# Kernel optimization log

Hardware: AMD Instinct MI355X
Metric: run time of the kernel (lower is better)

The kernel has to match this reference:

```python
import jax, jax.numpy as jnp
import numpy as np

B, OBS, ACT, NT, E, H1, H2, D = 4096, 390, 20, 10, 8, 1024, 512, 256


def setup_inputs() -> dict:
    key = jax.random.key(0)
    ks = jax.random.split(key, 16)
    f32 = jnp.float32

    def w(k, shape, fan_in):
        return jax.random.normal(k, shape, f32) / np.float32(np.sqrt(fan_in))

    return {
        "state_feat": jax.random.normal(ks[0], (B, OBS), f32),
        "act": jax.random.normal(ks[1], (B, ACT), f32),
        "task_id": jax.random.randint(ks[2], (B,), 0, NT, jnp.int32),
        "rep_W1": w(ks[3], (OBS + ACT, H1), OBS + ACT),
        "rep_b1": jnp.zeros((H1,), f32),
        "rep_W2": w(ks[4], (H1, H1), H1),
        "rep_b2": jnp.zeros((H1,), f32),
        "emb": 0.5 * jax.random.normal(ks[5], (NT, D), f32),
        "kW1": w(ks[6], (E, H1, H2), H1),
        "kb1": jnp.zeros((E, H2), f32),
        "kW2": w(ks[7], (E, H2, D), H2),
        "kb2": jnp.zeros((E, D), f32),
        "vW1": w(ks[8], (E, H1, H2), H1),
        "vb1": jnp.zeros((E, H2), f32),
        "vW2": w(ks[9], (E, H2, D), H2),
        "vb2": jnp.zeros((E, D), f32),
        "tW1": w(ks[10], (D, D), D),
        "tb1": jnp.zeros((D,), f32),
        "tW2": w(ks[11], (D, D), D),
        "tb2": jnp.zeros((D,), f32),
        "tW3": w(ks[12], (D, 1), D),
        "tb3": jnp.zeros((1,), f32),
    }


def reference(state_feat, act, task_id, rep_W1, rep_b1, rep_W2, rep_b2, emb,
              kW1, kb1, kW2, kb2, vW1, vb1, vW2, vb2,
              tW1, tb1, tW2, tb2, tW3, tb3):
    # representation: mlp([obs+act, 1024, 1024]) -> ReLU on first layer only
    x = jnp.concatenate([state_feat, act], axis=-1)              # [B, 410]
    rep = jnp.maximum(x @ rep_W1 + rep_b1, 0.0) @ rep_W2 + rep_b2  # [B, H1]
    query = jnp.tanh(emb[task_id])                               # [B, D]

    # batched per-expert key/value MLPs (grouped GEMM instead of python loop)
    hk = jnp.maximum(jnp.einsum('bi,eio->ebo', rep, kW1) + kb1[:, None, :], 0.0)
    keys = jnp.einsum('ebo,eod->ebd', hk, kW2) + kb2[:, None, :]   # [E, B, D]
    hv = jnp.maximum(jnp.einsum('bi,eio->ebo', rep, vW1) + vb1[:, None, :], 0.0)
    vals = jnp.einsum('ebo,eod->ebd', hv, vW2) + vb2[:, None, :]   # [E, B, D]

    scores = jnp.einsum('bd,ebd->be', query, keys)               # [B, E]
    weight = jax.nn.softmax(scores, axis=1)                      # [B, E]
    tower_in = jnp.einsum('be,ebd->bd', weight, vals)            # [B, D]

    # tower: mlp([256, 256, 256, 1]) -> ReLU, ReLU, Identity
    h = jnp.maximum(tower_in @ tW1 + tb1, 0.0)
    h = jnp.maximum(h @ tW2 + tb2, 0.0)
    q = (h @ tW3 + tb3)[:, 0]                                    # [B]

    expert_loss = -jnp.mean(
        jnp.sum(jnp.clip(jnp.log(weight + 1e-10), -6.0, 0.0), axis=-1) * 0.3)
    return q, expert_loss
```

## Files before the change

kernel.cpp:

```cpp
#include <hip/hip_runtime.h>

constexpr int Bn   = 4096;
constexpr int OBS  = 390;
constexpr int ACTN = 20;
constexpr int IN   = 410;
constexpr int KPAD = 448;
constexpr int E    = 8;
constexpr int NT   = 10;
constexpr int H1   = 1024;
constexpr int H2   = 512;
constexpr int D    = 256;

typedef __bf16 bf16x8 __attribute__((ext_vector_type(8)));
typedef float  f32x4  __attribute__((ext_vector_type(4)));
typedef unsigned short u16x8 __attribute__((ext_vector_type(8)));

__device__ __forceinline__ unsigned short f2bf(float f) {
    unsigned int u = __float_as_uint(f);
    unsigned int r = u + 0x7fffu + ((u >> 16) & 1u);
    return (unsigned short)(r >> 16);
}
__device__ __forceinline__ float bf2f(unsigned short h) {
    return __uint_as_float(((unsigned int)h) << 16);
}
__device__ __forceinline__ void gload16(void* lds_dst, const void* g_src) {
    __builtin_amdgcn_global_load_lds(
        (const __attribute__((address_space(1))) void*)g_src,
        (__attribute__((address_space(3))) void*)lds_dst,
        16, 0, 0);
}

struct TD2 {
    const float* W;
    unsigned short* WT;
    int K, Kpad, N;
    long long gsW, gsO;
    int tilesN, perG, start;
};
struct TD2Arr { TD2 d[8]; };

__global__ __launch_bounds__(256) void tc64(TD2Arr da) {
    int bid = blockIdx.x;
    int i = 0;
#pragma unroll
    for (int j = 1; j < 8; ++j) if (bid >= da.d[j].start) i = j;
    TD2 dd = da.d[i];
    int local = bid - dd.start;
    int g   = local / dd.perG;
    int rem = local - g * dd.perG;
    int kt  = rem / dd.tilesN;
    int nt  = rem - kt * dd.tilesN;
    const float* W = dd.W + (long long)g * dd.gsW;
    unsigned short* WT = dd.WT + (long long)g * dd.gsO;
    int k0 = kt * 64, n0 = nt * 64;

    __shared__ float tile[64][68];
    int t = threadIdx.x;
    {
        int kl  = t >> 4;
        int nl4 = (t & 15) * 4;
#pragma unroll
        for (int r = 0; r < 4; ++r) {
            int k = k0 + kl + r * 16;
            float4 v = make_float4(0.f, 0.f, 0.f, 0.f);
            if (k < dd.K) v = *(const float4*)(W + (long long)k * dd.N + n0 + nl4);
            *(float4*)&tile[kl + r * 16][nl4] = v;
        }
    }
    __syncthreads();
    int nl = t >> 2, kc = (t & 3) * 16;
    if (k0 + kc < dd.Kpad) {
        u16x8 o0, o1;
#pragma unroll
        for (int j = 0; j < 8; ++j) {
            o0[j] = f2bf(tile[kc + j][nl]);
            o1[j] = f2bf(tile[kc + 8 + j][nl]);
        }
        unsigned short* dst = WT + (long long)(n0 + nl) * dd.Kpad + k0 + kc;
        *(u16x8*)dst       = o0;
        *(u16x8*)(dst + 8) = o1;
    }
}

constexpr int PREPB = (Bn * KPAD) / 256;

__global__ __launch_bounds__(256) void misc_kernel(
    const float* __restrict__ sf, const float* __restrict__ ac,
    unsigned short* __restrict__ x,
    const float* __restrict__ kW2, const float* __restrict__ kb2,
    const float* __restrict__ emb, float* __restrict__ qp, float* __restrict__ qb,
    const float* __restrict__ kb1, const float* __restrict__ vb1,
    float* __restrict__ b1cat)
{
    int bid = blockIdx.x;
    if (bid < PREPB) {
        int idx = bid * 256 + threadIdx.x;
        int b = idx / KPAD;
        int k = idx - b * KPAD;
        float v = 0.f;
        if (k < OBS) v = sf[b * OBS + k];
        else if (k < IN) v = ac[b * ACTN + (k - OBS)];
        x[idx] = f2bf(v);
        return;
    }
    if (bid < PREPB + 17) {
        int qbid = bid - PREPB;
        __shared__ float tq[NT][D];
        for (int i = threadIdx.x; i < NT * D; i += 256)
            tq[i / D][i - (i / D) * D] = tanhf(emb[i]);
        __syncthreads();
        if (qbid < 16) {
            int e = qbid >> 1;
            int h = (qbid & 1) * 256 + threadIdx.x;
            const float4* row = (const float4*)(kW2 + ((long long)e * H2 + h) * D);
            float acc[NT] = {};
            for (int d4 = 0; d4 < D / 4; ++d4) {
                float4 wv = row[d4];
#pragma unroll
                for (int t = 0; t < NT; ++t)
                    acc[t] += wv.x * tq[t][d4 * 4] + wv.y * tq[t][d4 * 4 + 1]
                            + wv.z * tq[t][d4 * 4 + 2] + wv.w * tq[t][d4 * 4 + 3];
            }
#pragma unroll
            for (int t = 0; t < NT; ++t)
                qp[((long long)e * NT + t) * H2 + h] = acc[t];
        } else if (threadIdx.x < E * NT) {
            int e = threadIdx.x / NT, t = threadIdx.x - e * NT;
            float s = 0.f;
            for (int d = 0; d < D; ++d) s += kb2[e * D + d] * tq[t][d];
            qb[e * NT + t] = s;
        }
        return;
    }
    int i = (bid - PREPB - 17) * 256 + threadIdx.x;
    b1cat[i] = (i < E * H2) ? kb1[i] : vb1[i - E * H2];
}

template <int KT, int ACTF, int OUTF>
__global__ __launch_bounds__(256, 2) void gemm128p(
    const unsigned short* __restrict__ A, const unsigned short* __restrict__ BT,
    const float* __restrict__ bias, void* __restrict__ Cout,
    int ldc, long long gsA, long long gsBT, long long gsBias, long long gsC,
    const float* __restrict__ tW3 = nullptr, float* __restrict__ qpart = nullptr)
{
    constexpr int NTK = KT / 64;
    static_assert(NTK >= 2, "KT must be >= 128");

    const int g = blockIdx.z;
    A    += (long long)g * gsA;
    BT   += (long long)g * gsBT;
    bias += (long long)g * gsBias;
    float*          Cf = (float*)Cout + (long long)g * gsC;
    unsigned short* Cb = (unsigned short*)Cout + (long long)g * gsC;

    __shared__ __align__(16) char smem[65536];
    const int tid = threadIdx.x;
    const int l  = tid & 63, lr = l & 15, lk = l >> 4;
    const int w  = tid >> 6;
    const int wm = (w >> 1) * 64, wn = (w & 1) * 64;
    const int gm = blockIdx.y * 128, gn = blockIdx.x * 128;

    const int srow = tid >> 3;
    const int cg   = (tid & 7) ^ (srow & 7);
    const unsigned short* gA = A  + (long long)(gm + srow) * KT + cg * 8;
    const unsigned short* gB = BT + (long long)(gn + srow) * KT + cg * 8;
    const int wb = w * 1024;

    const int cs0 = ((0 | lk) ^ (lr & 7)) * 16;
    const int cs1 = ((4 | lk) ^ (lr & 7)) * 16;
    const int aRow = (wm + lr) * 128;
    const int bRow = 16384 + (wn + lr) * 128;

    f32x4 acc[4][4] = {};

    auto stA = [&](int c, int kt) {
#pragma unroll
        for (int j = 0; j < 4; ++j)
            gload16(smem + c * 32768 + j * 4096 + wb,
                    gA + (long long)(j * 32) * KT + kt * 64);
    };
    auto stB = [&](int c, int kt) {
#pragma unroll
        for (int j = 0; j < 4; ++j)
            gload16(smem + c * 32768 + 16384 + j * 4096 + wb,
                    gB + (long long)(j * 32) * KT + kt * 64);
    };

    stA(0, 0); stB(0, 0); stA(1, 1);
    asm volatile("s_waitcnt vmcnt(4)" ::: "memory");
    __builtin_amdgcn_s_barrier();
    __builtin_amdgcn_sched_barrier(0);

#pragma unroll
    for (int kt = 0; kt < NTK; ++kt) {
        const int c = kt & 1;
        const char* bufc = smem + c * 32768;
        bf16x8 a[4][2], b[2][2], b2[2][2];

#pragma unroll
        for (int m = 0; m < 4; ++m) {
            const char* base = bufc + aRow + m * 2048;
            a[m][0] = *(const bf16x8*)(base + cs0);
            a[m][1] = *(const bf16x8*)(base + cs1);
        }
#pragma unroll
        for (int n = 0; n < 2; ++n) {
            const char* base = bufc + bRow + n * 2048;
            b[n][0] = *(const bf16x8*)(base + cs0);
            b[n][1] = *(const bf16x8*)(base + cs1);
        }
        if (kt + 1 < NTK) stB(c ^ 1, kt + 1);
        __builtin_amdgcn_s_setprio(1);
#pragma unroll
        for (int ks = 0; ks < 2; ++ks)
#pragma unroll
            for (int m = 0; m < 4; ++m)
#pragma unroll
                for (int n = 0; n < 2; ++n)
                    acc[m][n] = __builtin_amdgcn_mfma_f32_16x16x32_bf16(
                        a[m][ks], b[n][ks], acc[m][n], 0, 0, 0);
        __builtin_amdgcn_s_setprio(0);

#pragma unroll
        for (int n = 0; n < 2; ++n) {
            const char* base = bufc + bRow + (2 + n) * 2048;
            b2[n][0] = *(const bf16x8*)(base + cs0);
            b2[n][1] = *(const bf16x8*)(base + cs1);
        }
        asm volatile("s_waitcnt lgkmcnt(0)" ::: "memory");
        __builtin_amdgcn_sched_barrier(0);
        if (kt + 2 < NTK) {
            __builtin_amdgcn_s_barrier();
            __builtin_amdgcn_sched_barrier(0);
            stA(c, kt + 2);
        }
        __builtin_amdgcn_s_setprio(1);
#pragma unroll
        for (int ks = 0; ks < 2; ++ks)
#pragma unroll
            for (int m = 0; m < 4; ++m)
#pragma unroll
                for (int n = 0; n < 2; ++n)
                    acc[m][2 + n] = __builtin_amdgcn_mfma_f32_16x16x32_bf16(
                        a[m][ks], b2[n][ks], acc[m][2 + n], 0, 0, 0);
        __builtin_amdgcn_s_setprio(0);

        if (kt + 1 < NTK) {
            if (kt + 2 < NTK) { asm volatile("s_waitcnt vmcnt(4)" ::: "memory"); }
            else              { asm volatile("s_waitcnt vmcnt(0)" ::: "memory"); }
            __builtin_amdgcn_sched_barrier(0);
            __builtin_amdgcn_s_barrier();
            __builtin_amdgcn_sched_barrier(0);
        }
    }

    const int orow0 = gm + wm + lk * 4;
    const int ocol0 = gn + wn + lr;
    float bv[4];
#pragma unroll
    for (int ni = 0; ni < 4; ++ni) bv[ni] = bias[gn + wn + lr + ni * 16];

    if (OUTF == 2) {
        float tw3v[4];
#pragma unroll
        for (int ni = 0; ni < 4; ++ni) tw3v[ni] = tW3[gn + wn + lr + ni * 16];
#pragma unroll
        for (int mi = 0; mi < 4; ++mi)
#pragma unroll
            for (int r = 0; r < 4; ++r) {
                float part = 0.f;
#pragma unroll
                for (int ni = 0; ni < 4; ++ni) {
                    float v = acc[mi][ni][r] + bv[ni];
                    if (ACTF == 1) v = fmaxf(v, 0.f);
                    part += v * tw3v[ni];
                }
                part += __shfl_xor(part, 1);
                part += __shfl_xor(part, 2);
                part += __shfl_xor(part, 4);
                part += __shfl_xor(part, 8);
                if (lr == 0)
                    qpart[(orow0 + mi * 16 + r) * 4 + ((wn >> 6) << 1) + blockIdx.x] = part;
            }
    } else {
#pragma unroll
        for (int mi = 0; mi < 4; ++mi)
#pragma unroll
            for (int ni = 0; ni < 4; ++ni)
#pragma unroll
                for (int r = 0; r < 4; ++r) {
                    float v = acc[mi][ni][r] + bv[ni];
                    if (ACTF == 1) v = fmaxf(v, 0.f);
                    long long off = (long long)(orow0 + mi * 16 + r) * ldc + ocol0 + ni * 16;
                    if (OUTF == 0) Cf[off] = v;
                    else           Cb[off] = f2bf(v);
                }
    }
}

template <int KTOT, int ACTF, int OUTF, int SC>
__global__ __launch_bounds__(512, 2) void gemm256(
    const unsigned short* __restrict__ A, const unsigned short* __restrict__ BT,
    const float* __restrict__ bias, void* __restrict__ Cout,
    int ldc, long long gsA, long long gsBT, long long gsBias, long long gsC,
    const int* __restrict__ task_id, const float* __restrict__ qp,
    float* __restrict__ spart)
{
    constexpr int NT_ = KTOT / 64;
    static_assert(NT_ >= 4 && (NT_ % 2) == 0, "KTOT must be multiple of 128");

    const int g = blockIdx.z;
    A    += (long long)g * gsA;
    BT   += (long long)g * gsBT;
    bias += (long long)g * gsBias;
    float*          Cf = (float*)Cout + (long long)g * gsC;
    unsigned short* Cb = (unsigned short*)Cout + (long long)g * gsC;

    __shared__ __align__(16) char smem[131072];

    const int tid = threadIdx.x;
    const int l  = tid & 63;
    const int lr = l & 15, lk = l >> 4;
    const int w  = tid >> 6;
    const int wr = w >> 2, wc = w & 3;
    const int gm = blockIdx.y * 256, gn = blockIdx.x * 256;

    const int srow = tid >> 3;
    const int cg   = (tid & 7) ^ (srow & 7);
    const unsigned short* gA = A  + (long long)(gm + srow) * KTOT + cg * 8;
    const unsigned short* gB = BT + (long long)(gn + srow) * KTOT + cg * 8;
    const int wbase = (tid & ~63) * 16;

    const int cs0 = ((0 | lk) ^ (lr & 7)) * 16;
    const int cs1 = ((4 | lk) ^ (lr & 7)) * 16;
    const int aRow = wr * 16384 + lr * 128;
    const int bRow = 32768 + (wc >> 1) * 16384 + ((wc & 1) * 64 + lr) * 128;

    f32x4 acc[8][4] = {};

    auto stA = [&](int c, int s, int kt) {
        const unsigned short* src = gA + (long long)(s * 128) * KTOT + kt * 64;
        char* d = smem + c * 65536 + s * 16384 + wbase;
        gload16(d,        src);
        gload16(d + 8192, src + (long long)64 * KTOT);
    };
    auto stB = [&](int c, int s, int kt) {
        const unsigned short* src = gB + (long long)(s * 128) * KTOT + kt * 64;
        char* d = smem + c * 65536 + 32768 + s * 16384 + wbase;
        gload16(d,        src);
        gload16(d + 8192, src + (long long)64 * KTOT);
    };

    stA(0, 0, 0); stA(0, 1, 0); stB(0, 0, 0); stB(0, 1, 0);
    stA(1, 0, 1); stA(1, 1, 1);
    asm volatile("s_waitcnt vmcnt(4)" ::: "memory");
    __builtin_amdgcn_s_barrier();
    __builtin_amdgcn_sched_barrier(0);

#pragma unroll
    for (int kt = 0; kt < NT_; ++kt) {
        const int c = kt & 1;
        const char* bufc = smem + c * 65536;
        bf16x8 a0[4], a1[4], b0[4], b1[4];

#pragma unroll
        for (int m = 0; m < 4; ++m) {
            const char* base = bufc + aRow + m * (16 * 128);
            a0[m] = *(const bf16x8*)(base + cs0);
            a1[m] = *(const bf16x8*)(base + cs1);
        }
#pragma unroll
        for (int n = 0; n < 4; ++n) {
            const char* base = bufc + bRow + n * (16 * 128);
            b0[n] = *(const bf16x8*)(base + cs0);
            b1[n] = *(const bf16x8*)(base + cs1);
        }
        if (kt + 1 < NT_) { stB(c ^ 1, 0, kt + 1); stB(c ^ 1, 1, kt + 1); }
        __builtin_amdgcn_s_setprio(1);
#pragma unroll
        for (int m = 0; m < 4; ++m)
#pragma unroll
            for (int n = 0; n < 4; ++n) {
                acc[m][n] = __builtin_amdgcn_mfma_f32_16x16x32_bf16(a0[m], b0[n], acc[m][n], 0, 0, 0);
                acc[m][n] = __builtin_amdgcn_mfma_f32_16x16x32_bf16(a1[m], b1[n], acc[m][n], 0, 0, 0);
            }
        __builtin_amdgcn_s_setprio(0);

#pragma unroll
        for (int m = 0; m < 4; ++m) {
            const char* base = bufc + aRow + (64 + m * 16) * 128;
            a0[m] = *(const bf16x8*)(base + cs0);
            a1[m] = *(const bf16x8*)(base + cs1);
        }
        asm volatile("s_waitcnt lgkmcnt(0)" ::: "memory");
        __builtin_amdgcn_sched_barrier(0);
        if (kt + 2 < NT_) {
            __builtin_amdgcn_s_barrier();
            __builtin_amdgcn_sched_barrier(0);
            stA(c, 0, kt + 2); stA(c, 1, kt + 2);
        }
        __builtin_amdgcn_s_setprio(1);
#pragma unroll
        for (int m = 0; m < 4; ++m)
#pragma unroll
            for (int n = 0; n < 4; ++n) {
                acc[4 + m][n] = __builtin_amdgcn_mfma_f32_16x16x32_bf16(a0[m], b0[n], acc[4 + m][n], 0, 0, 0);
                acc[4 + m][n] = __builtin_amdgcn_mfma_f32_16x16x32_bf16(a1[m], b1[n], acc[4 + m][n], 0, 0, 0);
            }
        __builtin_amdgcn_s_setprio(0);

        if (kt + 1 < NT_) {
            if (kt + 2 < NT_) { asm volatile("s_waitcnt vmcnt(4)" ::: "memory"); }
            else              { asm volatile("s_waitcnt vmcnt(0)" ::: "memory"); }
            __builtin_amdgcn_sched_barrier(0);
            __builtin_amdgcn_s_barrier();
            __builtin_amdgcn_sched_barrier(0);
        }
    }

    const int orow0 = gm + wr * 128 + lk * 4;
    const int ocol0 = gn + wc * 64 + lr;
    float bv[4];
#pragma unroll
    for (int ni = 0; ni < 4; ++ni) bv[ni] = bias[gn + wc * 64 + lr + ni * 16];

    if (SC && g < E) {
        __syncthreads();
        float* qpl  = (float*)smem;
        int*   tidl = (int*)(smem + NT * 256 * 4);
        for (int i = tid; i < NT * 256; i += 512) {
            int tt = i >> 8, cc = i & 255;
            qpl[i] = qp[((long long)(g * NT + tt)) * H2 + gn + cc];
        }
        if (tid < 256) tidl[tid] = task_id[gm + tid];
        __syncthreads();

        const int rbase = wr * 128 + lk * 4;
        const int cbase = wc * 64 + lr;
#pragma unroll
        for (int mi = 0; mi < 8; ++mi) {
#pragma unroll
            for (int r = 0; r < 4; ++r) {
                int trow = tidl[rbase + mi * 16 + r];
                float rp = 0.f;
#pragma unroll
                for (int ni = 0; ni < 4; ++ni) {
                    float v = acc[mi][ni][r] + bv[ni];
                    v = fmaxf(v, 0.f);
                    rp += v * qpl[trow * 256 + cbase + ni * 16];
                }
                rp += __shfl_xor(rp, 1);
                rp += __shfl_xor(rp, 2);
                rp += __shfl_xor(rp, 4);
                rp += __shfl_xor(rp, 8);
                if (lr == 0)
                    spart[(((long long)g * Bn + orow0 + mi * 16 + r) << 3)
                          + (wc << 1) + blockIdx.x] = rp;
            }
        }
    } else {
#pragma unroll
        for (int mi = 0; mi < 8; ++mi)
#pragma unroll
            for (int ni = 0; ni < 4; ++ni)
#pragma unroll
                for (int r = 0; r < 4; ++r) {
                    float v = acc[mi][ni][r] + bv[ni];
                    if (ACTF == 1) v = fmaxf(v, 0.f);
                    long long off = (long long)(orow0 + mi * 16 + r) * ldc + ocol0 + ni * 16;
                    if (OUTF == 0) Cf[off] = v;
                    else           Cb[off] = f2bf(v);
                }
    }
}

__global__ __launch_bounds__(256) void attn_kernel(
    const float* __restrict__ spart, const float* __restrict__ qb,
    const int* __restrict__ task_id, const unsigned short* __restrict__ vals,
    unsigned short* __restrict__ tower_in, float* __restrict__ loss_partial)
{
    int wv   = threadIdx.x >> 6;
    int lane = threadIdx.x & 63;
    int b    = blockIdx.x * 4 + wv;
    int t    = task_id[b];

    float s[E];
#pragma unroll
    for (int e = 0; e < E; ++e) {
        const float4* sp = (const float4*)(spart + (((long long)e * Bn + b) << 3));
        float4 p0 = sp[0], p1 = sp[1];
        s[e] = p0.x + p0.y + p0.z + p0.w + p1.x + p1.y + p1.z + p1.w + qb[e * NT + t];
    }

    float m = s[0];
#pragma unroll
    for (int e = 1; e < E; ++e) m = fmaxf(m, s[e]);
    float wgt[E];
    float sum = 0.f;
#pragma unroll
    for (int e = 0; e < E; ++e) { wgt[e] = expf(s[e] - m); sum += wgt[e]; }
    float inv = 1.f / sum;

    int d0 = lane * 4;
    float4 acc = make_float4(0.f, 0.f, 0.f, 0.f);
    float lb = 0.f;
#pragma unroll
    for (int e = 0; e < E; ++e) {
        float we = wgt[e] * inv;
        uint2 vv = *(const uint2*)&vals[((long long)e * Bn + b) * D + d0];
        acc.x += we * __uint_as_float(vv.x << 16);
        acc.y += we * __uint_as_float(vv.x & 0xffff0000u);
        acc.z += we * __uint_as_float(vv.y << 16);
        acc.w += we * __uint_as_float(vv.y & 0xffff0000u);
        lb += fminf(fmaxf(logf(we + 1e-10f), -6.f), 0.f);
    }
    ushort4 o;
    o.x = f2bf(acc.x); o.y = f2bf(acc.y); o.z = f2bf(acc.z); o.w = f2bf(acc.w);
    *(ushort4*)&tower_in[(long long)b * D + d0] = o;

    __shared__ float sm[4];
    if (lane == 0) sm[wv] = lb;
    __syncthreads();
    if (threadIdx.x == 0)
        loss_partial[blockIdx.x] = sm[0] + sm[1] + sm[2] + sm[3];
}

__global__ __launch_bounds__(256) void qfin_kernel(
    const float* __restrict__ qpart, const float* __restrict__ tb3,
    float* __restrict__ out, const float* __restrict__ lossp)
{
    if (blockIdx.x == Bn / 256) {
        float s = 0.f;
        for (int i = threadIdx.x; i < Bn / 4; i += 256) s += lossp[i];
#pragma unroll
        for (int off = 32; off > 0; off >>= 1) s += __shfl_xor(s, off, 64);
        __shared__ float sm[4];
        if ((threadIdx.x & 63) == 0) sm[threadIdx.x >> 6] = s;
        __syncthreads();
        if (threadIdx.x == 0) out[Bn] = (-0.3f / Bn) * (sm[0] + sm[1] + sm[2] + sm[3]);
        return;
    }
    int b = blockIdx.x * 256 + threadIdx.x;
    float4 qpv = *(const float4*)&qpart[b * 4];
    out[b] = qpv.x + qpv.y + qpv.z + qpv.w + tb3[0];
}

extern "C" void kernel_launch(void* const* d_in, const int* in_sizes, int n_in,
                              void* d_out, int out_size, void* d_ws, size_t ws_size,
                              hipStream_t stream) {
    const float* state_feat = (const float*)d_in[0];
    const float* act        = (const float*)d_in[1];
    const int*   task_id    = (const int*)d_in[2];
    const float* rep_W1 = (const float*)d_in[3];
    const float* rep_b1 = (const float*)d_in[4];
    const float* rep_W2 = (const float*)d_in[5];
    const float* rep_b2 = (const float*)d_in[6];
    const float* emb    = (const float*)d_in[7];
    const float* kW1 = (const float*)d_in[8];
    const float* kb1 = (const float*)d_in[9];
    const float* kW2 = (const float*)d_in[10];
    const float* kb2 = (const float*)d_in[11];
    const float* vW1 = (const float*)d_in[12];
    const float* vb1 = (const float*)d_in[13];
    const float* vW2 = (const float*)d_in[14];
    const float* vb2 = (const float*)d_in[15];
    const float* tW1 = (const float*)d_in[16];
    const float* tb1 = (const float*)d_in[17];
    const float* tW2 = (const float*)d_in[18];
    const float* tb2 = (const float*)d_in[19];
    const float* tW3 = (const float*)d_in[20];
    const float* tb3 = (const float*)d_in[21];
    float* out = (float*)d_out;

    char* p = (char*)d_ws;
    auto alloc = [&](size_t bytes) {
        char* r = p;
        p += (bytes + 255) & ~(size_t)255;
        return r;
    };
    unsigned short* x      = (unsigned short*)alloc((size_t)Bn * KPAD * 2);
    unsigned short* repW1T = (unsigned short*)alloc((size_t)H1 * KPAD * 2);
    unsigned short* repW2T = (unsigned short*)alloc((size_t)H1 * H1 * 2);
    unsigned short* w1T    = (unsigned short*)alloc((size_t)2 * E * H2 * H1 * 2);
    unsigned short* w2T    = (unsigned short*)alloc((size_t)E * D * H2 * 2);
    unsigned short* tW1T   = (unsigned short*)alloc((size_t)D * D * 2);
    unsigned short* tW2T   = (unsigned short*)alloc((size_t)D * D * 2);
    float*          b1cat  = (float*)alloc((size_t)2 * E * H2 * 4);
    float*          qp     = (float*)alloc((size_t)E * NT * H2 * 4);
    float*          qb     = (float*)alloc((size_t)E * NT * 4);
    char*           h1zone = alloc((size_t)Bn * H1 * 2);
    unsigned short* rep    = (unsigned short*)alloc((size_t)Bn * H1 * 2);
    unsigned short* hkv    = (unsigned short*)alloc((size_t)2 * E * Bn * H2 * 2);
    unsigned short* vals   = (unsigned short*)alloc((size_t)E * Bn * D * 2);
    float*          spart  = (float*)alloc((size_t)E * Bn * 8 * 4);
    float*          qpart  = (float*)alloc((size_t)Bn * 4 * 4);
    float*          lossp  = (float*)alloc((size_t)(Bn / 4) * 4);

    unsigned short* h1       = (unsigned short*)h1zone;
    unsigned short* tower_in = (unsigned short*)h1zone;
    unsigned short* t1       = (unsigned short*)(h1zone + (size_t)Bn * D * 2);
    unsigned short* hv = hkv + (size_t)E * Bn * H2;

    TD2Arr da;
    int startAcc = 0;
    auto setd = [&](int i, const float* W, unsigned short* WT, int K, int Kpad, int N,
                    long long gsW, long long gsO, int groups) {
        TD2& dd = da.d[i];
        dd.W = W; dd.WT = WT; dd.K = K; dd.Kpad = Kpad; dd.N = N;
        dd.gsW = gsW; dd.gsO = gsO;
        dd.tilesN = N / 64;
        dd.perG = ((Kpad + 63) / 64) * dd.tilesN;
        dd.start = startAcc;
        startAcc += dd.perG * groups;
    };
    setd(0, rep_W1, repW1T, IN, KPAD, H1, 0, 0, 1);
    setd(1, rep_W2, repW2T, H1, H1, H1, 0, 0, 1);
    setd(2, kW1, w1T,                       H1, H1, H2, (long long)H1 * H2, (long long)H2 * H1, E);
    setd(3, vW1, w1T + (size_t)E * H2 * H1, H1, H1, H2, (long long)H1 * H2, (long long)H2 * H1, E);
    setd(4, vW2, w2T,                       H2, H2, D, (long long)H2 * D, (long long)D * H2, E);
    setd(5, tW1, tW1T, D, D, D, 0, 0, 1);
    setd(6, tW2, tW2T, D, D, D, 0, 0, 1);
    da.d[7] = da.d[6];
    da.d[7].start = 0x7fffffff;
    tc64<<<startAcc, 256, 0, stream>>>(da);

    misc_kernel<<<PREPB + 17 + 32, 256, 0, stream>>>(
        state_feat, act, x, kW2, kb2, emb, qp, qb, kb1, vb1, b1cat);

    gemm128p<KPAD, 1, 1><<<dim3(H1 / 128, Bn / 128, 1), 256, 0, stream>>>(
        x, repW1T, rep_b1, h1, H1, 0, 0, 0, 0);
    gemm128p<H1, 0, 1><<<dim3(H1 / 128, Bn / 128, 1), 256, 0, stream>>>(
        h1, repW2T, rep_b2, rep, H1, 0, 0, 0, 0);

    gemm256<H1, 1, 1, 1><<<dim3(H2 / 256, Bn / 256, 2 * E), 512, 0, stream>>>(
        rep, w1T, b1cat, hkv, H2,
        0, (long long)H2 * H1, H2, (long long)Bn * H2,
        task_id, qp, spart);
    gemm128p<H2, 0, 1><<<dim3(D / 128, Bn / 128, E), 256, 0, stream>>>(
        hv, w2T, vb2, vals, D,
        (long long)Bn * H2, (long long)D * H2, D, (long long)Bn * D);

    attn_kernel<<<Bn / 4, 256, 0, stream>>>(
        spart, qb, task_id, vals, tower_in, lossp);

    gemm128p<D, 1, 1><<<dim3(D / 128, Bn / 128, 1), 256, 0, stream>>>(
        tower_in, tW1T, tb1, t1, D, 0, 0, 0, 0);
    gemm128p<D, 1, 2><<<dim3(D / 128, Bn / 128, 1), 256, 0, stream>>>(
        t1, tW2T, tb2, nullptr, D, 0, 0, 0, 0, tW3, qpart);

    qfin_kernel<<<Bn / 256 + 1, 256, 0, stream>>>(qpart, tb3, out, lossp);
}
```

Baseline: 162.3 us.

## Merge prep kernels, shrink GEMM tiles to 64x128, restructure B prefetch

Merges the weight transpose/convert kernel and the misc prep kernel into one launch to save a launch and a serialization point. Replaces the 128x128 GEMM with a 64x128 tile (each wave owns 32 columns) at 3 blocks per CU, doubling the grid for the small GEMMs so more CUs have work. Both GEMM kernels now prefetch A and B two stages ahead together instead of loading B one stage ahead, which changes the wait counts. The tower epilogue now writes 8 partial sums per row, and the final reduction is widened to match. The price is less data reuse per tile and more LDS traffic per MFMA.

```diff
diff --git a/kernel.cpp b/kernel.cpp
--- a/kernel.cpp
+++ b/kernel.cpp
@@ -39,52 +39,10 @@
 };
 struct TD2Arr { TD2 d[8]; };
 
-__global__ __launch_bounds__(256) void tc64(TD2Arr da) {
-    int bid = blockIdx.x;
-    int i = 0;
-#pragma unroll
-    for (int j = 1; j < 8; ++j) if (bid >= da.d[j].start) i = j;
-    TD2 dd = da.d[i];
-    int local = bid - dd.start;
-    int g   = local / dd.perG;
-    int rem = local - g * dd.perG;
-    int kt  = rem / dd.tilesN;
-    int nt  = rem - kt * dd.tilesN;
-    const float* W = dd.W + (long long)g * dd.gsW;
-    unsigned short* WT = dd.WT + (long long)g * dd.gsO;
-    int k0 = kt * 64, n0 = nt * 64;
-
-    __shared__ float tile[64][68];
-    int t = threadIdx.x;
-    {
-        int kl  = t >> 4;
-        int nl4 = (t & 15) * 4;
-#pragma unroll
-        for (int r = 0; r < 4; ++r) {
-            int k = k0 + kl + r * 16;
-            float4 v = make_float4(0.f, 0.f, 0.f, 0.f);
-            if (k < dd.K) v = *(const float4*)(W + (long long)k * dd.N + n0 + nl4);
-            *(float4*)&tile[kl + r * 16][nl4] = v;
-        }
-    }
-    __syncthreads();
-    int nl = t >> 2, kc = (t & 3) * 16;
-    if (k0 + kc < dd.Kpad) {
-        u16x8 o0, o1;
-#pragma unroll
-        for (int j = 0; j < 8; ++j) {
-            o0[j] = f2bf(tile[kc + j][nl]);
-            o1[j] = f2bf(tile[kc + 8 + j][nl]);
-        }
-        unsigned short* dst = WT + (long long)(n0 + nl) * dd.Kpad + k0 + kc;
-        *(u16x8*)dst       = o0;
-        *(u16x8*)(dst + 8) = o1;
-    }
-}
-
 constexpr int PREPB = (Bn * KPAD) / 256;
 
-__global__ __launch_bounds__(256) void misc_kernel(
+__global__ __launch_bounds__(256) void prep_all(
+    TD2Arr da, int tcb,
     const float* __restrict__ sf, const float* __restrict__ ac,
     unsigned short* __restrict__ x,
     const float* __restrict__ kW2, const float* __restrict__ kb2,
@@ -92,9 +50,52 @@
     const float* __restrict__ kb1, const float* __restrict__ vb1,
     float* __restrict__ b1cat)
 {
+    __shared__ float tile[64][68];
     int bid = blockIdx.x;
-    if (bid < PREPB) {
-        int idx = bid * 256 + threadIdx.x;
+    int t = threadIdx.x;
+
+    if (bid < tcb) {
+        int i = 0;
+#pragma unroll
+        for (int j = 1; j < 8; ++j) if (bid >= da.d[j].start) i = j;
+        TD2 dd = da.d[i];
+        int local = bid - dd.start;
+        int g   = local / dd.perG;
+        int rem = local - g * dd.perG;
+        int kt  = rem / dd.tilesN;
+        int nt  = rem - kt * dd.tilesN;
+        const float* W = dd.W + (long long)g * dd.gsW;
+        unsigned short* WT = dd.WT + (long long)g * dd.gsO;
+        int k0 = kt * 64, n0 = nt * 64;
+        {
+            int kl  = t >> 4;
+            int nl4 = (t & 15) * 4;
+#pragma unroll
+            for (int r = 0; r < 4; ++r) {
+                int k = k0 + kl + r * 16;
+                float4 v = make_float4(0.f, 0.f, 0.f, 0.f);
+                if (k < dd.K) v = *(const float4*)(W + (long long)k * dd.N + n0 + nl4);
+                *(float4*)&tile[kl + r * 16][nl4] = v;
+            }
+        }
+        __syncthreads();
+        int nl = t >> 2, kc = (t & 3) * 16;
+        if (k0 + kc < dd.Kpad) {
+            u16x8 o0, o1;
+#pragma unroll
+            for (int j = 0; j < 8; ++j) {
+                o0[j] = f2bf(tile[kc + j][nl]);
+                o1[j] = f2bf(tile[kc + 8 + j][nl]);
+            }
+            unsigned short* dst = WT + (long long)(n0 + nl) * dd.Kpad + k0 + kc;
+            *(u16x8*)dst       = o0;
+            *(u16x8*)(dst + 8) = o1;
+        }
+        return;
+    }
+    int bid2 = bid - tcb;
+    if (bid2 < PREPB) {
+        int idx = bid2 * 256 + t;
         int b = idx / KPAD;
         int k = idx - b * KPAD;
         float v = 0.f;
@@ -103,41 +104,40 @@
         x[idx] = f2bf(v);
         return;
     }
-    if (bid < PREPB + 17) {
-        int qbid = bid - PREPB;
-        __shared__ float tq[NT][D];
-        for (int i = threadIdx.x; i < NT * D; i += 256)
-            tq[i / D][i - (i / D) * D] = tanhf(emb[i]);
+    if (bid2 < PREPB + 17) {
+        int qbid = bid2 - PREPB;
+        float* tq = &tile[0][0];
+        for (int i = t; i < NT * D; i += 256) tq[i] = tanhf(emb[i]);
         __syncthreads();
         if (qbid < 16) {
             int e = qbid >> 1;
-            int h = (qbid & 1) * 256 + threadIdx.x;
+            int h = (qbid & 1) * 256 + t;
             const float4* row = (const float4*)(kW2 + ((long long)e * H2 + h) * D);
             float acc[NT] = {};
             for (int d4 = 0; d4 < D / 4; ++d4) {
                 float4 wv = row[d4];
 #pragma unroll
-                for (int t = 0; t < NT; ++t)
-                    acc[t] += wv.x * tq[t][d4 * 4] + wv.y * tq[t][d4 * 4 + 1]
-                            + wv.z * tq[t][d4 * 4 + 2] + wv.w * tq[t][d4 * 4 + 3];
+                for (int tt = 0; tt < NT; ++tt)
+                    acc[tt] += wv.x * tq[tt * D + d4 * 4] + wv.y * tq[tt * D + d4 * 4 + 1]
+                             + wv.z * tq[tt * D + d4 * 4 + 2] + wv.w * tq[tt * D + d4 * 4 + 3];
             }
 #pragma unroll
-            for (int t = 0; t < NT; ++t)
-                qp[((long long)e * NT + t) * H2 + h] = acc[t];
-        } else if (threadIdx.x < E * NT) {
-            int e = threadIdx.x / NT, t = threadIdx.x - e * NT;
+            for (int tt = 0; tt < NT; ++tt)
+                qp[((long long)e * NT + tt) * H2 + h] = acc[tt];
+        } else if (t < E * NT) {
+            int e = t / NT, tt = t - e * NT;
             float s = 0.f;
-            for (int d = 0; d < D; ++d) s += kb2[e * D + d] * tq[t][d];
-            qb[e * NT + t] = s;
+            for (int d = 0; d < D; ++d) s += kb2[e * D + d] * tq[tt * D + d];
+            qb[e * NT + tt] = s;
         }
         return;
     }
-    int i = (bid - PREPB - 17) * 256 + threadIdx.x;
+    int i = (bid2 - PREPB - 17) * 256 + t;
     b1cat[i] = (i < E * H2) ? kb1[i] : vb1[i - E * H2];
 }
 
 template <int KT, int ACTF, int OUTF>
-__global__ __launch_bounds__(256, 2) void gemm128p(
+__global__ __launch_bounds__(256, 3) void gemm64x128(
     const unsigned short* __restrict__ A, const unsigned short* __restrict__ BT,
     const float* __restrict__ bias, void* __restrict__ Cout,
     int ldc, long long gsA, long long gsBT, long long gsBias, long long gsC,
@@ -153,12 +153,11 @@
     float*          Cf = (float*)Cout + (long long)g * gsC;
     unsigned short* Cb = (unsigned short*)Cout + (long long)g * gsC;
 
-    __shared__ __align__(16) char smem[65536];
+    __shared__ __align__(16) char smem[49152];
     const int tid = threadIdx.x;
     const int l  = tid & 63, lr = l & 15, lk = l >> 4;
     const int w  = tid >> 6;
-    const int wm = (w >> 1) * 64, wn = (w & 1) * 64;
-    const int gm = blockIdx.y * 128, gn = blockIdx.x * 128;
+    const int gm = blockIdx.y * 64, gn = blockIdx.x * 128;
 
     const int srow = tid >> 3;
     const int cg   = (tid & 7) ^ (srow & 7);
@@ -168,34 +167,34 @@
 
     const int cs0 = ((0 | lk) ^ (lr & 7)) * 16;
     const int cs1 = ((4 | lk) ^ (lr & 7)) * 16;
-    const int aRow = (wm + lr) * 128;
-    const int bRow = 16384 + (wn + lr) * 128;
-
-    f32x4 acc[4][4] = {};
+    const int aRow = lr * 128;
+    const int bRow = 8192 + (w * 32 + lr) * 128;
+
+    f32x4 acc[4][2] = {};
 
     auto stA = [&](int c, int kt) {
 #pragma unroll
-        for (int j = 0; j < 4; ++j)
-            gload16(smem + c * 32768 + j * 4096 + wb,
+        for (int j = 0; j < 2; ++j)
+            gload16(smem + c * 24576 + j * 4096 + wb,
                     gA + (long long)(j * 32) * KT + kt * 64);
     };
     auto stB = [&](int c, int kt) {
 #pragma unroll
         for (int j = 0; j < 4; ++j)
-            gload16(smem + c * 32768 + 16384 + j * 4096 + wb,
+            gload16(smem + c * 24576 + 8192 + j * 4096 + wb,
                     gB + (long long)(j * 32) * KT + kt * 64);
     };
 
-    stA(0, 0); stB(0, 0); stA(1, 1);
-    asm volatile("s_waitcnt vmcnt(4)" ::: "memory");
+    stA(0, 0); stB(0, 0); stA(1, 1); stB(1, 1);
+    asm volatile("s_waitcnt vmcnt(6)" ::: "memory");
     __builtin_amdgcn_s_barrier();
     __builtin_amdgcn_sched_barrier(0);
 
 #pragma unroll
     for (int kt = 0; kt < NTK; ++kt) {
         const int c = kt & 1;
-        const char* bufc = smem + c * 32768;
-        bf16x8 a[4][2], b[2][2], b2[2][2];
+        const char* bufc = smem + c * 24576;
+        bf16x8 a[4][2], b[1][2], b2[1][2];
 
 #pragma unroll
         for (int m = 0; m < 4; ++m) {
@@ -203,50 +202,43 @@
             a[m][0] = *(const bf16x8*)(base + cs0);
             a[m][1] = *(const bf16x8*)(base + cs1);
         }
-#pragma unroll
-        for (int n = 0; n < 2; ++n) {
-            const char* base = bufc + bRow + n * 2048;
-            b[n][0] = *(const bf16x8*)(base + cs0);
-            b[n][1] = *(const bf16x8*)(base + cs1);
-        }
-        if (kt + 1 < NTK) stB(c ^ 1, kt + 1);
+        {
+            const char* base = bufc + bRow;
+            b[0][0] = *(const bf16x8*)(base + cs0);
+            b[0][1] = *(const bf16x8*)(base + cs1);
+        }
         __builtin_amdgcn_s_setprio(1);
 #pragma unroll
         for (int ks = 0; ks < 2; ++ks)
 #pragma unroll
             for (int m = 0; m < 4; ++m)
-#pragma unroll
-                for (int n = 0; n < 2; ++n)
-                    acc[m][n] = __builtin_amdgcn_mfma_f32_16x16x32_bf16(
-                        a[m][ks], b[n][ks], acc[m][n], 0, 0, 0);
+                acc[m][0] = __builtin_amdgcn_mfma_f32_16x16x32_bf16(
+                    a[m][ks], b[0][ks], acc[m][0], 0, 0, 0);
         __builtin_amdgcn_s_setprio(0);
 
-#pragma unroll
-        for (int n = 0; n < 2; ++n) {
-            const char* base = bufc + bRow + (2 + n) * 2048;
-            b2[n][0] = *(const bf16x8*)(base + cs0);
-            b2[n][1] = *(const bf16x8*)(base + cs1);
+        {
+            const char* base = bufc + bRow + 2048;
+            b2[0][0] = *(const bf16x8*)(base + cs0);
+            b2[0][1] = *(const bf16x8*)(base + cs1);
         }
         asm volatile("s_waitcnt lgkmcnt(0)" ::: "memory");
         __builtin_amdgcn_sched_barrier(0);
         if (kt + 2 < NTK) {
             __builtin_amdgcn_s_barrier();
             __builtin_amdgcn_sched_barrier(0);
-            stA(c, kt + 2);
+            stA(c, kt + 2); stB(c, kt + 2);
         }
         __builtin_amdgcn_s_setprio(1);
 #pragma unroll
         for (int ks = 0; ks < 2; ++ks)
 #pragma unroll
             for (int m = 0; m < 4; ++m)
-#pragma unroll
-                for (int n = 0; n < 2; ++n)
-                    acc[m][2 + n] = __builtin_amdgcn_mfma_f32_16x16x32_bf16(
-                        a[m][ks], b2[n][ks], acc[m][2 + n], 0, 0, 0);
+                acc[m][1] = __builtin_amdgcn_mfma_f32_16x16x32_bf16(
+                    a[m][ks], b2[0][ks], acc[m][1], 0, 0, 0);
         __builtin_amdgcn_s_setprio(0);
 
         if (kt + 1 < NTK) {
-            if (kt + 2 < NTK) { asm volatile("s_waitcnt vmcnt(4)" ::: "memory"); }
+            if (kt + 2 < NTK) { asm volatile("s_waitcnt vmcnt(6)" ::: "memory"); }
             else              { asm volatile("s_waitcnt vmcnt(0)" ::: "memory"); }
             __builtin_amdgcn_sched_barrier(0);
             __builtin_amdgcn_s_barrier();
@@ -254,44 +246,44 @@
         }
     }
 
-    const int orow0 = gm + wm + lk * 4;
-    const int ocol0 = gn + wn + lr;
-    float bv[4];
-#pragma unroll
-    for (int ni = 0; ni < 4; ++ni) bv[ni] = bias[gn + wn + lr + ni * 16];
+    const int orow0 = gm + lk * 4;
+    const int ocol0 = gn + w * 32 + lr;
+    float bv[2];
+#pragma unroll
+    for (int nf = 0; nf < 2; ++nf) bv[nf] = bias[gn + w * 32 + lr + nf * 16];
 
     if (OUTF == 2) {
-        float tw3v[4];
-#pragma unroll
-        for (int ni = 0; ni < 4; ++ni) tw3v[ni] = tW3[gn + wn + lr + ni * 16];
+        float tw3v[2];
+#pragma unroll
+        for (int nf = 0; nf < 2; ++nf) tw3v[nf] = tW3[gn + w * 32 + lr + nf * 16];
 #pragma unroll
         for (int mi = 0; mi < 4; ++mi)
 #pragma unroll
             for (int r = 0; r < 4; ++r) {
                 float part = 0.f;
 #pragma unroll
-                for (int ni = 0; ni < 4; ++ni) {
-                    float v = acc[mi][ni][r] + bv[ni];
+                for (int nf = 0; nf < 2; ++nf) {
+                    float v = acc[mi][nf][r] + bv[nf];
                     if (ACTF == 1) v = fmaxf(v, 0.f);
-                    part += v * tw3v[ni];
+                    part += v * tw3v[nf];
                 }
                 part += __shfl_xor(part, 1);
                 part += __shfl_xor(part, 2);
                 part += __shfl_xor(part, 4);
                 part += __shfl_xor(part, 8);
                 if (lr == 0)
-                    qpart[(orow0 + mi * 16 + r) * 4 + ((wn >> 6) << 1) + blockIdx.x] = part;
+                    qpart[(orow0 + mi * 16 + r) * 8 + blockIdx.x * 4 + w] = part;
             }
     } else {
 #pragma unroll
         for (int mi = 0; mi < 4; ++mi)
 #pragma unroll
-            for (int ni = 0; ni < 4; ++ni)
+            for (int nf = 0; nf < 2; ++nf)
 #pragma unroll
                 for (int r = 0; r < 4; ++r) {
-                    float v = acc[mi][ni][r] + bv[ni];
+                    float v = acc[mi][nf][r] + bv[nf];
                     if (ACTF == 1) v = fmaxf(v, 0.f);
-                    long long off = (long long)(orow0 + mi * 16 + r) * ldc + ocol0 + ni * 16;
+                    long long off = (long long)(orow0 + mi * 16 + r) * ldc + ocol0 + nf * 16;
                     if (OUTF == 0) Cf[off] = v;
                     else           Cb[off] = f2bf(v);
                 }
@@ -352,8 +344,8 @@
     };
 
     stA(0, 0, 0); stA(0, 1, 0); stB(0, 0, 0); stB(0, 1, 0);
-    stA(1, 0, 1); stA(1, 1, 1);
-    asm volatile("s_waitcnt vmcnt(4)" ::: "memory");
+    stA(1, 0, 1); stA(1, 1, 1); stB(1, 0, 1); stB(1, 1, 1);
+    asm volatile("s_waitcnt vmcnt(8)" ::: "memory");
     __builtin_amdgcn_s_barrier();
     __builtin_amdgcn_sched_barrier(0);
 
@@ -375,7 +367,6 @@
             b0[n] = *(const bf16x8*)(base + cs0);
             b1[n] = *(const bf16x8*)(base + cs1);
         }
-        if (kt + 1 < NT_) { stB(c ^ 1, 0, kt + 1); stB(c ^ 1, 1, kt + 1); }
         __builtin_amdgcn_s_setprio(1);
 #pragma unroll
         for (int m = 0; m < 4; ++m)
@@ -398,6 +389,7 @@
             __builtin_amdgcn_s_barrier();
             __builtin_amdgcn_sched_barrier(0);
             stA(c, 0, kt + 2); stA(c, 1, kt + 2);
+            stB(c, 0, kt + 2); stB(c, 1, kt + 2);
         }
         __builtin_amdgcn_s_setprio(1);
 #pragma unroll
@@ -410,7 +402,7 @@
         __builtin_amdgcn_s_setprio(0);
 
         if (kt + 1 < NT_) {
-            if (kt + 2 < NT_) { asm volatile("s_waitcnt vmcnt(4)" ::: "memory"); }
+            if (kt + 2 < NT_) { asm volatile("s_waitcnt vmcnt(8)" ::: "memory"); }
             else              { asm volatile("s_waitcnt vmcnt(0)" ::: "memory"); }
             __builtin_amdgcn_sched_barrier(0);
             __builtin_amdgcn_s_barrier();
@@ -541,8 +533,9 @@
         return;
     }
     int b = blockIdx.x * 256 + threadIdx.x;
-    float4 qpv = *(const float4*)&qpart[b * 4];
-    out[b] = qpv.x + qpv.y + qpv.z + qpv.w + tb3[0];
+    const float4* qq = (const float4*)&qpart[b * 8];
+    float4 a0 = qq[0], a1 = qq[1];
+    out[b] = a0.x + a0.y + a0.z + a0.w + a1.x + a1.y + a1.z + a1.w + tb3[0];
 }
 
 extern "C" void kernel_launch(void* const* d_in, const int* in_sizes, int n_in,
@@ -593,7 +586,7 @@
     unsigned short* hkv    = (unsigned short*)alloc((size_t)2 * E * Bn * H2 * 2);
     unsigned short* vals   = (unsigned short*)alloc((size_t)E * Bn * D * 2);
     float*          spart  = (float*)alloc((size_t)E * Bn * 8 * 4);
-    float*          qpart  = (float*)alloc((size_t)Bn * 4 * 4);
+    float*          qpart  = (float*)alloc((size_t)Bn * 8 * 4);
     float*          lossp  = (float*)alloc((size_t)(Bn / 4) * 4);
 
     unsigned short* h1       = (unsigned short*)h1zone;
@@ -622,30 +615,29 @@
     setd(6, tW2, tW2T, D, D, D, 0, 0, 1);
     da.d[7] = da.d[6];
     da.d[7].start = 0x7fffffff;
-    tc64<<<startAcc, 256, 0, stream>>>(da);
-
-    misc_kernel<<<PREPB + 17 + 32, 256, 0, stream>>>(
-        state_feat, act, x, kW2, kb2, emb, qp, qb, kb1, vb1, b1cat);
-
-    gemm128p<KPAD, 1, 1><<<dim3(H1 / 128, Bn / 128, 1), 256, 0, stream>>>(
+    int totalBlocks = startAcc + PREPB + 17 + 32;
+    prep_all<<<totalBlocks, 256, 0, stream>>>(
+        da, startAcc, state_feat, act, x, kW2, kb2, emb, qp, qb, kb1, vb1, b1cat);
+
+    gemm64x128<KPAD, 1, 1><<<dim3(H1 / 128, Bn / 64, 1), 256, 0, stream>>>(
         x, repW1T, rep_b1, h1, H1, 0, 0, 0, 0);
-    gemm128p<H1, 0, 1><<<dim3(H1 / 128, Bn / 128, 1), 256, 0, stream>>>(
+    gemm64x128<H1, 0, 1><<<dim3(H1 / 128, Bn / 64, 1), 256, 0, stream>>>(
         h1, repW2T, rep_b2, rep, H1, 0, 0, 0, 0);
 
     gemm256<H1, 1, 1, 1><<<dim3(H2 / 256, Bn / 256, 2 * E), 512, 0, stream>>>(
         rep, w1T, b1cat, hkv, H2,
         0, (long long)H2 * H1, H2, (long long)Bn * H2,
         task_id, qp, spart);
-    gemm128p<H2, 0, 1><<<dim3(D / 128, Bn / 128, E), 256, 0, stream>>>(
+    gemm64x128<H2, 0, 1><<<dim3(D / 128, Bn / 64, E), 256, 0, stream>>>(
         hv, w2T, vb2, vals, D,
         (long long)Bn * H2, (long long)D * H2, D, (long long)Bn * D);
 
     attn_kernel<<<Bn / 4, 256, 0, stream>>>(
         spart, qb, task_id, vals, tower_in, lossp);
 
-    gemm128p<D, 1, 1><<<dim3(D / 128, Bn / 128, 1), 256, 0, stream>>>(
+    gemm64x128<D, 1, 1><<<dim3(D / 128, Bn / 64, 1), 256, 0, stream>>>(
         tower_in, tW1T, tb1, t1, D, 0, 0, 0, 0);
-    gemm128p<D, 1, 2><<<dim3(D / 128, Bn / 128, 1), 256, 0, stream>>>(
+    gemm64x128<D, 1, 2><<<dim3(D / 128, Bn / 64, 1), 256, 0, stream>>>(
         t1, tW2T, tb2, nullptr, D, 0, 0, 0, 0, tW3, qpart);
 
     qfin_kernel<<<Bn / 256 + 1, 256, 0, stream>>>(qpart, tb3, out, lossp);
```

After: 160.0 us. Within noise of the previous version (-1.4%).
